# Performance work log

Hardware: AMD Instinct MI355X
Metric: run time of the kernel (lower is better)

## Reference

```python
import jax, jax.numpy as jnp
import numpy as np

DIM = 512
HEADS = 8
DIM_HEAD = 64
INNER = HEADS * DIM_HEAD  # 512
SCALE = DIM_HEAD ** -0.5
NEG = -jnp.finfo(jnp.float32).max


def setup_inputs() -> dict:
    key = jax.random.key(0)
    k1, k2, k3, k4, k5 = jax.random.split(key, 5)
    b, n = 2, 4096
    x = jax.random.normal(k1, (b, n, DIM), dtype=jnp.float32)
    mask = jnp.ones((b, n), dtype=bool)
    gamma = jnp.ones((DIM,), dtype=jnp.float32)
    # nn.Linear default init ~ U(-1/sqrt(fan_in), 1/sqrt(fan_in)); use scaled normal for simplicity
    Wq = jax.random.normal(k2, (DIM, INNER), dtype=jnp.float32) * (DIM ** -0.5)
    Wkv = jax.random.normal(k3, (DIM, 2 * INNER), dtype=jnp.float32) * (DIM ** -0.5)
    Wout = jax.random.normal(k4, (INNER, DIM), dtype=jnp.float32) * (INNER ** -0.5)
    return {"x": x, "mask": mask, "gamma": gamma, "Wq": Wq, "Wkv": Wkv, "Wout": Wout}


def _layer_norm(x, gamma):
    mu = jnp.mean(x, axis=-1, keepdims=True)
    var = jnp.var(x, axis=-1, keepdims=True)
    return (x - mu) * jax.lax.rsqrt(var + 1e-5) * gamma  # beta buffer is zeros


def reference(x, mask, gamma, Wq, Wkv, Wout):
    b, n, _ = x.shape
    xn = _layer_norm(x, gamma)
    q = xn @ Wq                      # [b,n,inner]
    kv = xn @ Wkv                    # [b,n,2*inner]
    k, v = jnp.split(kv, 2, axis=-1)
    # b n (h d) -> b h n d
    def split_heads(t):
        return t.reshape(b, n, HEADS, DIM_HEAD).transpose(0, 2, 1, 3)
    q, k, v = split_heads(q) * SCALE, split_heads(k), split_heads(v)
    sim = jnp.einsum('bhid,bhjd->bhij', q, k)  # [b,h,n,n]
    sim = jnp.where(mask[:, None, None, :], sim, NEG)
    causal = jnp.triu(jnp.ones((n, n), dtype=bool), k=1)
    sim = jnp.where(causal, NEG, sim)
    attn = jax.nn.softmax(sim, axis=-1)
    out = jnp.einsum('bhij,bhjd->bhid', attn, v)       # [b,h,n,d]
    out = out.transpose(0, 2, 1, 3).reshape(b, n, INNER)
    return out @ Wout
```

## Files before the change

kernel.cpp:

```cpp
#include <hip/hip_runtime.h>
#include <hip/hip_bf16.h>
#include <stdint.h>

typedef __attribute__((ext_vector_type(8))) short bf16x8;
typedef __attribute__((ext_vector_type(4))) short s16x4;
typedef __attribute__((ext_vector_type(4))) float f32x4;
typedef __attribute__((ext_vector_type(16))) float f32x16;
typedef __attribute__((ext_vector_type(4))) uint32_t u32x4;

__device__ __forceinline__ short f2bf(float f) {
    union { float f; uint32_t u; } v; v.f = f;
    uint32_t r = v.u + 0x7fffu + ((v.u >> 16) & 1u);
    return (short)(r >> 16);
}

__device__ __forceinline__ float bf2f(uint32_t bits) {
    union { uint32_t u; float f; } v; v.u = bits;
    return v.f;
}

__device__ __forceinline__ uint32_t cvtpk(float a, float b) {
    uint32_t r;
    asm("v_cvt_pk_bf16_f32 %0, %1, %2" : "=v"(r) : "v"(a), "v"(b));
    return r;
}

__device__ __forceinline__ void plswap(uint32_t& x, uint32_t& y) {
    asm volatile("v_permlane32_swap_b32 %0, %1" : "+v"(x), "+v"(y));
}

__device__ __forceinline__ f32x16 mfma32(bf16x8 a, bf16x8 b, f32x16 c) {
    return __builtin_amdgcn_mfma_f32_32x32x16_bf16(a, b, c, 0, 0, 0);
}

__device__ __forceinline__ void gload_lds16(const void* g, void* l) {
    __builtin_amdgcn_global_load_lds(
        (const __attribute__((address_space(1))) void*)g,
        (__attribute__((address_space(3))) void*)l, 16, 0, 0);
}

__global__ __launch_bounds__(256) void prep_ln(
    const float* __restrict__ x, const float* __restrict__ gamma,
    const float* __restrict__ Wq, const float* __restrict__ Wkv,
    const float* __restrict__ Wout, short* __restrict__ xn,
    short* __restrict__ WqkvT, short* __restrict__ WoutT) {
    if (blockIdx.x < 8192) {
        int row = blockIdx.x;
        const float* xr = x + (size_t)row * 512;
        float2 v = *(const float2*)(xr + threadIdx.x * 2);
        float s = v.x + v.y;
        float ss = v.x * v.x + v.y * v.y;
#pragma unroll
        for (int off = 1; off < 64; off <<= 1) {
            s += __shfl_xor(s, off);
            ss += __shfl_xor(ss, off);
        }
        __shared__ float sbuf[4], ssbuf[4];
        int wid = threadIdx.x >> 6;
        if ((threadIdx.x & 63) == 0) { sbuf[wid] = s; ssbuf[wid] = ss; }
        __syncthreads();
        s = sbuf[0] + sbuf[1] + sbuf[2] + sbuf[3];
        ss = ssbuf[0] + ssbuf[1] + ssbuf[2] + ssbuf[3];
        float mu = s * (1.f / 512.f);
        float var = ss * (1.f / 512.f) - mu * mu;
        float rstd = rsqrtf(var + 1e-5f);
        float2 g = *(const float2*)(gamma + threadIdx.x * 2);
        uint32_t lo = (uint16_t)f2bf((v.x - mu) * rstd * g.x);
        uint32_t hi = (uint16_t)f2bf((v.y - mu) * rstd * g.y);
        *(uint32_t*)(xn + (size_t)row * 512 + threadIdx.x * 2) = lo | (hi << 16);
    } else {
        int tid = (blockIdx.x - 8192) * 256 + threadIdx.x;
        if (tid < 1536 * 512) {
            int n = tid >> 9, k = tid & 511;
            float w = (n < 512) ? Wq[k * 512 + n] : Wkv[k * 1024 + (n - 512)];
            WqkvT[tid] = f2bf(w);
        } else {
            int t = tid - 1536 * 512;
            int n = t >> 9, k = t & 511;
            WoutT[t] = f2bf(Wout[k * 512 + n]);
        }
    }
}

template <int EPI>
__global__ __launch_bounds__(256) void gemm_bt(const short* __restrict__ A,
                                               const short* __restrict__ Bt,
                                               void* __restrict__ C,
                                               short* __restrict__ Vt) {
    constexpr int K = 512;
    __shared__ __align__(16) short As[128 * 64];
    __shared__ __align__(16) short Bs[128 * 64];
    const int tid = threadIdx.x;
    const int lane = tid & 63;
    const int wid = tid >> 6;
    const int m0 = blockIdx.x * 128;
    const int n0 = blockIdx.y * 128;
    const int wr = wid >> 1, wc = wid & 1;
    const int hi = lane >> 4, lo = lane & 15;

    f32x4 acc[4][4] = {};
    for (int kt = 0; kt < K / 64; ++kt) {
        __syncthreads();
#pragma unroll
        for (int r = 0; r < 4; ++r) {
            int c = (r * 4 + wid) * 64 + lane;
            int row = c >> 3, c8 = c & 7;
            int kcol = kt * 64 + ((c8 ^ (row & 7)) << 3);
            gload_lds16(A + (size_t)(m0 + row) * K + kcol,
                        (char*)As + (r * 4 + wid) * 1024);
            gload_lds16(Bt + (size_t)(n0 + row) * K + kcol,
                        (char*)Bs + (r * 4 + wid) * 1024);
        }
        __syncthreads();
#pragma unroll
        for (int kk = 0; kk < 2; ++kk) {
            bf16x8 af[4], bfr[4];
            int cc = hi + kk * 4;
#pragma unroll
            for (int i = 0; i < 4; ++i) {
                int row = wr * 64 + i * 16 + lo;
                af[i] = *(const bf16x8*)((const char*)As + row * 128 +
                                         ((cc ^ (row & 7)) << 4));
                int nrow = wc * 64 + i * 16 + lo;
                bfr[i] = *(const bf16x8*)((const char*)Bs + nrow * 128 +
                                          ((cc ^ (nrow & 7)) << 4));
            }
#pragma unroll
            for (int i = 0; i < 4; ++i)
#pragma unroll
                for (int j = 0; j < 4; ++j)
                    acc[i][j] = __builtin_amdgcn_mfma_f32_16x16x32_bf16(
                        af[i], bfr[j], acc[i][j], 0, 0, 0);
        }
    }
#pragma unroll
    for (int i = 0; i < 4; ++i)
#pragma unroll
        for (int j = 0; j < 4; ++j) {
            int col = n0 + wc * 64 + j * 16 + lo;
            int row0 = m0 + wr * 64 + i * 16 + hi * 4;
            if (EPI == 1) {
#pragma unroll
                for (int r = 0; r < 4; ++r)
                    ((float*)C)[(size_t)(row0 + r) * 512 + col] = acc[i][j][r];
            } else if (col < 1024) {
                float sc = (col < 512) ? 0.18033688011112042f : 1.0f;
#pragma unroll
                for (int r = 0; r < 4; ++r)
                    ((short*)C)[(size_t)(row0 + r) * 1536 + col] =
                        f2bf(acc[i][j][r] * sc);
            } else {
                s16x4 pk;
#pragma unroll
                for (int r = 0; r < 4; ++r) pk[r] = f2bf(acc[i][j][r]);
                int d = col - 1024;
                int bb = row0 >> 12, n = row0 & 4095;
                *(s16x4*)(Vt + ((size_t)(bb * 8 + (d >> 6)) * 64 + (d & 63)) *
                                   4096 +
                          n) = pk;
            }
        }
}

__global__ __launch_bounds__(256, 4) void flash_attn(
    const short* __restrict__ qkv, const short* __restrict__ Vt,
    short* __restrict__ attn_out) {
    __shared__ __align__(16) char smem[32768];
    const int tid = threadIdx.x, lane = tid & 63, w = tid >> 6;
    const int hi32 = lane >> 5, lq = lane & 31;
    const int bid = blockIdx.x;
    const int qt = 127 - (bid >> 4);
    const int bh = bid & 15, b = bh >> 3, h = bh & 7;
    const int q0 = qt * 32;
    const int qg = q0 + lq;
    const int swzK = (lq & 7) ^ ((lq >> 3) & 1);
    const int swzV = (lq >> 1) & 3;

    bf16x8 qb[4];
    {
        const short* qrow = qkv + (size_t)(b * 4096 + qg) * 1536 + h * 64;
#pragma unroll
        for (int ks = 0; ks < 4; ++ks)
            qb[ks] = *(const bf16x8*)(qrow + ks * 16 + hi32 * 8);
    }

    int offK[4], offV[4], ldsO[4];
#pragma unroll
    for (int r = 0; r < 4; ++r) {
        int idx = r * 64 + lane;
        int krow = idx >> 3, kc = idx & 7;
        int ksw = (krow & 7) ^ ((krow >> 3) & 1);
        offK[r] = krow * 1536 + ((kc ^ ksw) << 3);
        int vrow = idx >> 2, vc = idx & 3;
        offV[r] = vrow * 4096 + ((vc ^ ((vrow >> 1) & 3)) << 3);
        ldsO[r] = idx * 16;
    }
    char* mybuf = smem + w * 8192;
    const short* kps =
        qkv + (size_t)b * 4096 * 1536 + 512 + h * 64 + (size_t)w * 32 * 1536;
    const short* vps = Vt + (size_t)bh * 64 * 4096 + w * 32;

    f32x16 oA = {}, oB = {};
    float m_r = -3.0e38f, l_r = 0.f;
    const int T = qt + 1;

    if (w < T) {
#pragma unroll
        for (int r = 0; r < 4; ++r) {
            gload_lds16(kps + offK[r], mybuf + ldsO[r]);
            gload_lds16(vps + offV[r], mybuf + 4096 + ldsO[r]);
        }
        kps += (size_t)4 * 32 * 1536;
        vps += 4 * 32;
        for (int t = w; t < T; t += 4) {
            asm volatile("s_waitcnt vmcnt(0)" ::: "memory");
            f32x16 sA = {};
            __builtin_amdgcn_s_setprio(1);
#pragma unroll
            for (int ks = 0; ks < 4; ++ks) {
                int p = (2 * ks + hi32) ^ swzK;
                bf16x8 kf = *(const bf16x8*)(mybuf + lq * 128 + p * 16);
                sA = mfma32(kf, qb[ks], sA);
            }
            __builtin_amdgcn_s_setprio(0);
            bf16x8 vfA[2], vfB[2];
#pragma unroll
            for (int ks = 0; ks < 2; ++ks) {
                int p = (2 * ks + hi32) ^ swzV;
                vfA[ks] = *(const bf16x8*)(mybuf + 4096 + lq * 64 + p * 16);
                vfB[ks] =
                    *(const bf16x8*)(mybuf + 4096 + (lq + 32) * 64 + p * 16);
            }
            asm volatile("s_waitcnt lgkmcnt(0)" ::: "memory");
            __builtin_amdgcn_sched_barrier(0);
            if (t + 4 < T) {
#pragma unroll
                for (int r = 0; r < 4; ++r) {
                    gload_lds16(kps + offK[r], mybuf + ldsO[r]);
                    gload_lds16(vps + offV[r], mybuf + 4096 + ldsO[r]);
                }
                kps += (size_t)4 * 32 * 1536;
                vps += 4 * 32;
            }
            int kv0 = t * 32;
            if (kv0 + 31 > q0) {
                int c4 = 4 * hi32;
#pragma unroll
                for (int r2 = 0; r2 < 16; ++r2) {
                    int kvl = (r2 & 3) + 8 * (r2 >> 2) + c4;
                    sA[r2] = (kv0 + kvl > qg) ? -3.0e38f : sA[r2];
                }
            }
            float a0 = fmaxf(fmaxf(sA[0], sA[1]), sA[2]);
            float a1 = fmaxf(fmaxf(sA[3], sA[4]), sA[5]);
            float a2 = fmaxf(fmaxf(sA[6], sA[7]), sA[8]);
            float a3 = fmaxf(fmaxf(sA[9], sA[10]), sA[11]);
            float a4 = fmaxf(fmaxf(sA[12], sA[13]), sA[14]);
            float mt = fmaxf(fmaxf(fmaxf(a0, a1), a2),
                             fmaxf(fmaxf(a3, a4), sA[15]));
            mt = fmaxf(mt, __shfl_xor(mt, 32));
            if (!__all(mt <= m_r + 8.0f)) {
                float alpha = exp2f(m_r - mt);
                m_r = mt;
                l_r *= alpha;
#pragma unroll
                for (int r2 = 0; r2 < 16; ++r2) {
                    oA[r2] *= alpha;
                    oB[r2] *= alpha;
                }
            }
#pragma unroll
            for (int r2 = 0; r2 < 16; ++r2) sA[r2] = exp2f(sA[r2] - m_r);
            float sum0;
            {
                float s0 = (sA[0] + sA[1]) + (sA[2] + sA[3]);
                float s1 = (sA[4] + sA[5]) + (sA[6] + sA[7]);
                float s2 = (sA[8] + sA[9]) + (sA[10] + sA[11]);
                float s3 = (sA[12] + sA[13]) + (sA[14] + sA[15]);
                sum0 = (s0 + s1) + (s2 + s3);
            }
            l_r += sum0 + __shfl_xor(sum0, 32);
#pragma unroll
            for (int ks = 0; ks < 2; ++ks) {
                const int base = ks * 8;
                uint32_t x0 = cvtpk(sA[base + 0], sA[base + 1]);
                uint32_t y0 = cvtpk(sA[base + 4], sA[base + 5]);
                plswap(x0, y0);
                uint32_t x1 = cvtpk(sA[base + 2], sA[base + 3]);
                uint32_t y1 = cvtpk(sA[base + 6], sA[base + 7]);
                plswap(x1, y1);
                union { uint32_t wd[4]; bf16x8 v; } u;
                u.wd[0] = x0; u.wd[1] = x1; u.wd[2] = y0; u.wd[3] = y1;
                __builtin_amdgcn_s_setprio(1);
                oA = mfma32(vfA[ks], u.v, oA);
                oB = mfma32(vfB[ks], u.v, oB);
                __builtin_amdgcn_s_setprio(0);
            }
        }
    }
    __syncthreads();
    {
        char* epi = smem + w * 4224;
        float invl = (l_r > 0.f) ? (1.0f / l_r) : 0.f;
#pragma unroll
        for (int r2 = 0; r2 < 16; r2 += 2) {
            int wbase = ((r2 & 3) >> 1) + 4 * (r2 >> 2) + 2 * hi32;
            *(uint32_t*)(epi + lq * 132 + wbase * 4) =
                cvtpk(oA[r2] * invl, oA[r2 + 1] * invl);
            *(uint32_t*)(epi + lq * 132 + 64 + wbase * 4) =
                cvtpk(oB[r2] * invl, oB[r2 + 1] * invl);
        }
        float* mlb = (float*)(smem + 16896);
        if (hi32 == 0) {
            mlb[w * 64 + lq] = m_r;
            mlb[w * 64 + 32 + lq] = l_r;
        }
    }
    __syncthreads();
    {
        const int q = tid >> 3, dg = tid & 7;
        const float* mlb = (const float*)(smem + 16896);
        float M = -3.0e38f;
        float mm[4], ll[4];
#pragma unroll
        for (int s = 0; s < 4; ++s) {
            mm[s] = mlb[s * 64 + q];
            ll[s] = mlb[s * 64 + 32 + q];
            M = fmaxf(M, mm[s]);
        }
        float L = 0.f;
        float acc[8] = {};
#pragma unroll
        for (int s = 0; s < 4; ++s) {
            float a = exp2f(mm[s] - M) * ll[s];
            L += a;
            const uint32_t* p32 =
                (const uint32_t*)(smem + s * 4224 + q * 132 + dg * 16);
#pragma unroll
            for (int j = 0; j < 4; ++j) {
                uint32_t pv = p32[j];
                acc[2 * j] += a * bf2f(pv << 16);
                acc[2 * j + 1] += a * bf2f(pv & 0xffff0000u);
            }
        }
        float inv = 1.0f / L;
        u32x4 o;
#pragma unroll
        for (int j = 0; j < 4; ++j)
            o[j] = cvtpk(acc[2 * j] * inv, acc[2 * j + 1] * inv);
        uint32_t* attn32 = (uint32_t*)attn_out;
        *(u32x4*)(attn32 + (size_t)(b * 4096 + q0 + q) * 256 + h * 32 + dg * 4) =
            o;
    }
}

extern "C" void kernel_launch(void* const* d_in, const int* in_sizes, int n_in,
                              void* d_out, int out_size, void* d_ws,
                              size_t ws_size, hipStream_t stream) {
    const float* x = (const float*)d_in[0];
    const float* gamma = (const float*)d_in[2];
    const float* Wq = (const float*)d_in[3];
    const float* Wkv = (const float*)d_in[4];
    const float* Wout = (const float*)d_in[5];

    char* ws = (char*)d_ws;
    short* xn = (short*)(ws);
    short* qkv = (short*)(ws + (8ull << 20));
    short* Vt = (short*)(ws + (32ull << 20));
    short* attn = (short*)(ws + (40ull << 20));
    short* WqkvT = (short*)(ws + (48ull << 20));
    short* WoutT = (short*)(ws + (50ull << 20));

    prep_ln<<<12288, 256, 0, stream>>>(x, gamma, Wq, Wkv, Wout, xn, WqkvT,
                                       WoutT);
    gemm_bt<0><<<dim3(64, 12), 256, 0, stream>>>(xn, WqkvT, qkv, Vt);
    flash_attn<<<2048, 256, 0, stream>>>(qkv, Vt, attn);
    gemm_bt<1><<<dim3(64, 4), 256, 0, stream>>>(attn, WoutT, (float*)d_out,
                                                nullptr);
}
```

Measured before the change: 130.8 us.

## Process two 32-row query tiles per flash-attention block to reuse K/V loads

Each attention block now handles 64 query rows as two 32-row sub-tiles sharing every K/V tile staged in LDS. This halves the block count and the global K/V traffic per query. The price is more accumulator registers, so the launch-bounds occupancy hint drops from 4 to 3, and a two-phase epilogue is added. The first sub-tile skips fully masked KV tiles.

```diff
diff --git a/kernel.cpp b/kernel.cpp
--- a/kernel.cpp
+++ b/kernel.cpp
@@ -162,26 +162,28 @@
         }
 }
 
-__global__ __launch_bounds__(256, 4) void flash_attn(
+__global__ __launch_bounds__(256, 3) void flash_attn(
     const short* __restrict__ qkv, const short* __restrict__ Vt,
     short* __restrict__ attn_out) {
     __shared__ __align__(16) char smem[32768];
     const int tid = threadIdx.x, lane = tid & 63, w = tid >> 6;
     const int hi32 = lane >> 5, lq = lane & 31;
     const int bid = blockIdx.x;
-    const int qt = 127 - (bid >> 4);
+    const int s = 63 - (bid >> 4);
     const int bh = bid & 15, b = bh >> 3, h = bh & 7;
-    const int q0 = qt * 32;
-    const int qg = q0 + lq;
+    const int q0 = s * 64;
+    const int qgA = q0 + lq;
     const int swzK = (lq & 7) ^ ((lq >> 3) & 1);
     const int swzV = (lq >> 1) & 3;
 
-    bf16x8 qb[4];
+    bf16x8 qbA[4], qbB[4];
     {
-        const short* qrow = qkv + (size_t)(b * 4096 + qg) * 1536 + h * 64;
-#pragma unroll
-        for (int ks = 0; ks < 4; ++ks)
-            qb[ks] = *(const bf16x8*)(qrow + ks * 16 + hi32 * 8);
+        const short* qrowA = qkv + (size_t)(b * 4096 + qgA) * 1536 + h * 64;
+#pragma unroll
+        for (int ks = 0; ks < 4; ++ks) {
+            qbA[ks] = *(const bf16x8*)(qrowA + ks * 16 + hi32 * 8);
+            qbB[ks] = *(const bf16x8*)(qrowA + 32 * 1536 + ks * 16 + hi32 * 8);
+        }
     }
 
     int offK[4], offV[4], ldsO[4];
@@ -200,9 +202,10 @@
         qkv + (size_t)b * 4096 * 1536 + 512 + h * 64 + (size_t)w * 32 * 1536;
     const short* vps = Vt + (size_t)bh * 64 * 4096 + w * 32;
 
-    f32x16 oA = {}, oB = {};
-    float m_r = -3.0e38f, l_r = 0.f;
-    const int T = qt + 1;
+    f32x16 oAA = {}, oBA = {};
+    f32x16 oAB = {}, oBB = {};
+    float mA = -3.0e38f, lA = 0.f, mB = -3.0e38f, lB = 0.f;
+    const int T = 2 * s + 2;
 
     if (w < T) {
 #pragma unroll
@@ -213,14 +216,17 @@
         kps += (size_t)4 * 32 * 1536;
         vps += 4 * 32;
         for (int t = w; t < T; t += 4) {
+            const int kv0 = t * 32;
+            const bool doA = kv0 <= q0 + 31;
             asm volatile("s_waitcnt vmcnt(0)" ::: "memory");
-            f32x16 sA = {};
+            f32x16 sA = {}, sB = {};
             __builtin_amdgcn_s_setprio(1);
 #pragma unroll
             for (int ks = 0; ks < 4; ++ks) {
                 int p = (2 * ks + hi32) ^ swzK;
                 bf16x8 kf = *(const bf16x8*)(mybuf + lq * 128 + p * 16);
-                sA = mfma32(kf, qb[ks], sA);
+                sA = mfma32(kf, qbA[ks], sA);
+                sB = mfma32(kf, qbB[ks], sB);
             }
             __builtin_amdgcn_s_setprio(0);
             bf16x8 vfA[2], vfB[2];
@@ -242,115 +248,173 @@
                 kps += (size_t)4 * 32 * 1536;
                 vps += 4 * 32;
             }
-            int kv0 = t * 32;
-            if (kv0 + 31 > q0) {
-                int c4 = 4 * hi32;
-#pragma unroll
-                for (int r2 = 0; r2 < 16; ++r2) {
-                    int kvl = (r2 & 3) + 8 * (r2 >> 2) + c4;
-                    sA[r2] = (kv0 + kvl > qg) ? -3.0e38f : sA[r2];
-                }
-            }
-            float a0 = fmaxf(fmaxf(sA[0], sA[1]), sA[2]);
-            float a1 = fmaxf(fmaxf(sA[3], sA[4]), sA[5]);
-            float a2 = fmaxf(fmaxf(sA[6], sA[7]), sA[8]);
-            float a3 = fmaxf(fmaxf(sA[9], sA[10]), sA[11]);
-            float a4 = fmaxf(fmaxf(sA[12], sA[13]), sA[14]);
-            float mt = fmaxf(fmaxf(fmaxf(a0, a1), a2),
-                             fmaxf(fmaxf(a3, a4), sA[15]));
-            mt = fmaxf(mt, __shfl_xor(mt, 32));
-            if (!__all(mt <= m_r + 8.0f)) {
-                float alpha = exp2f(m_r - mt);
-                m_r = mt;
-                l_r *= alpha;
-#pragma unroll
-                for (int r2 = 0; r2 < 16; ++r2) {
-                    oA[r2] *= alpha;
-                    oB[r2] *= alpha;
-                }
-            }
-#pragma unroll
-            for (int r2 = 0; r2 < 16; ++r2) sA[r2] = exp2f(sA[r2] - m_r);
-            float sum0;
-            {
+            if (doA) {
+                if (kv0 + 31 > q0) {
+                    int c4 = 4 * hi32;
+#pragma unroll
+                    for (int r2 = 0; r2 < 16; ++r2) {
+                        int kvl = (r2 & 3) + 8 * (r2 >> 2) + c4;
+                        sA[r2] = (kv0 + kvl > qgA) ? -3.0e38f : sA[r2];
+                    }
+                }
+                float a0 = fmaxf(fmaxf(sA[0], sA[1]), sA[2]);
+                float a1 = fmaxf(fmaxf(sA[3], sA[4]), sA[5]);
+                float a2 = fmaxf(fmaxf(sA[6], sA[7]), sA[8]);
+                float a3 = fmaxf(fmaxf(sA[9], sA[10]), sA[11]);
+                float a4 = fmaxf(fmaxf(sA[12], sA[13]), sA[14]);
+                float mt = fmaxf(fmaxf(fmaxf(a0, a1), a2),
+                                 fmaxf(fmaxf(a3, a4), sA[15]));
+                mt = fmaxf(mt, __shfl_xor(mt, 32));
+                if (!__all(mt <= mA + 8.0f)) {
+                    float alpha = exp2f(mA - mt);
+                    mA = mt;
+                    lA *= alpha;
+#pragma unroll
+                    for (int r2 = 0; r2 < 16; ++r2) {
+                        oAA[r2] *= alpha;
+                        oBA[r2] *= alpha;
+                    }
+                }
+#pragma unroll
+                for (int r2 = 0; r2 < 16; ++r2) sA[r2] = exp2f(sA[r2] - mA);
                 float s0 = (sA[0] + sA[1]) + (sA[2] + sA[3]);
                 float s1 = (sA[4] + sA[5]) + (sA[6] + sA[7]);
                 float s2 = (sA[8] + sA[9]) + (sA[10] + sA[11]);
                 float s3 = (sA[12] + sA[13]) + (sA[14] + sA[15]);
-                sum0 = (s0 + s1) + (s2 + s3);
-            }
-            l_r += sum0 + __shfl_xor(sum0, 32);
-#pragma unroll
-            for (int ks = 0; ks < 2; ++ks) {
-                const int base = ks * 8;
-                uint32_t x0 = cvtpk(sA[base + 0], sA[base + 1]);
-                uint32_t y0 = cvtpk(sA[base + 4], sA[base + 5]);
-                plswap(x0, y0);
-                uint32_t x1 = cvtpk(sA[base + 2], sA[base + 3]);
-                uint32_t y1 = cvtpk(sA[base + 6], sA[base + 7]);
-                plswap(x1, y1);
-                union { uint32_t wd[4]; bf16x8 v; } u;
-                u.wd[0] = x0; u.wd[1] = x1; u.wd[2] = y0; u.wd[3] = y1;
-                __builtin_amdgcn_s_setprio(1);
-                oA = mfma32(vfA[ks], u.v, oA);
-                oB = mfma32(vfB[ks], u.v, oB);
-                __builtin_amdgcn_s_setprio(0);
-            }
-        }
-    }
-    __syncthreads();
-    {
-        char* epi = smem + w * 4224;
-        float invl = (l_r > 0.f) ? (1.0f / l_r) : 0.f;
-#pragma unroll
-        for (int r2 = 0; r2 < 16; r2 += 2) {
-            int wbase = ((r2 & 3) >> 1) + 4 * (r2 >> 2) + 2 * hi32;
-            *(uint32_t*)(epi + lq * 132 + wbase * 4) =
-                cvtpk(oA[r2] * invl, oA[r2 + 1] * invl);
-            *(uint32_t*)(epi + lq * 132 + 64 + wbase * 4) =
-                cvtpk(oB[r2] * invl, oB[r2 + 1] * invl);
-        }
-        float* mlb = (float*)(smem + 16896);
-        if (hi32 == 0) {
-            mlb[w * 64 + lq] = m_r;
-            mlb[w * 64 + 32 + lq] = l_r;
-        }
-    }
-    __syncthreads();
-    {
-        const int q = tid >> 3, dg = tid & 7;
-        const float* mlb = (const float*)(smem + 16896);
-        float M = -3.0e38f;
-        float mm[4], ll[4];
-#pragma unroll
-        for (int s = 0; s < 4; ++s) {
-            mm[s] = mlb[s * 64 + q];
-            ll[s] = mlb[s * 64 + 32 + q];
-            M = fmaxf(M, mm[s]);
-        }
-        float L = 0.f;
-        float acc[8] = {};
-#pragma unroll
-        for (int s = 0; s < 4; ++s) {
-            float a = exp2f(mm[s] - M) * ll[s];
-            L += a;
-            const uint32_t* p32 =
-                (const uint32_t*)(smem + s * 4224 + q * 132 + dg * 16);
-#pragma unroll
-            for (int j = 0; j < 4; ++j) {
-                uint32_t pv = p32[j];
-                acc[2 * j] += a * bf2f(pv << 16);
-                acc[2 * j + 1] += a * bf2f(pv & 0xffff0000u);
-            }
-        }
-        float inv = 1.0f / L;
-        u32x4 o;
-#pragma unroll
-        for (int j = 0; j < 4; ++j)
-            o[j] = cvtpk(acc[2 * j] * inv, acc[2 * j + 1] * inv);
-        uint32_t* attn32 = (uint32_t*)attn_out;
-        *(u32x4*)(attn32 + (size_t)(b * 4096 + q0 + q) * 256 + h * 32 + dg * 4) =
-            o;
+                float sum0 = (s0 + s1) + (s2 + s3);
+                lA += sum0 + __shfl_xor(sum0, 32);
+#pragma unroll
+                for (int ks = 0; ks < 2; ++ks) {
+                    const int base = ks * 8;
+                    uint32_t x0 = cvtpk(sA[base + 0], sA[base + 1]);
+                    uint32_t y0 = cvtpk(sA[base + 4], sA[base + 5]);
+                    plswap(x0, y0);
+                    uint32_t x1 = cvtpk(sA[base + 2], sA[base + 3]);
+                    uint32_t y1 = cvtpk(sA[base + 6], sA[base + 7]);
+                    plswap(x1, y1);
+                    union { uint32_t wd[4]; bf16x8 v; } u;
+                    u.wd[0] = x0; u.wd[1] = x1; u.wd[2] = y0; u.wd[3] = y1;
+                    __builtin_amdgcn_s_setprio(1);
+                    oAA = mfma32(vfA[ks], u.v, oAA);
+                    oBA = mfma32(vfB[ks], u.v, oBA);
+                    __builtin_amdgcn_s_setprio(0);
+                }
+            }
+            {
+                if (kv0 + 31 > q0 + 32) {
+                    int c4 = 4 * hi32;
+#pragma unroll
+                    for (int r2 = 0; r2 < 16; ++r2) {
+                        int kvl = (r2 & 3) + 8 * (r2 >> 2) + c4;
+                        sB[r2] = (kv0 + kvl > qgA + 32) ? -3.0e38f : sB[r2];
+                    }
+                }
+                float a0 = fmaxf(fmaxf(sB[0], sB[1]), sB[2]);
+                float a1 = fmaxf(fmaxf(sB[3], sB[4]), sB[5]);
+                float a2 = fmaxf(fmaxf(sB[6], sB[7]), sB[8]);
+                float a3 = fmaxf(fmaxf(sB[9], sB[10]), sB[11]);
+                float a4 = fmaxf(fmaxf(sB[12], sB[13]), sB[14]);
+                float mt = fmaxf(fmaxf(fmaxf(a0, a1), a2),
+                                 fmaxf(fmaxf(a3, a4), sB[15]));
+                mt = fmaxf(mt, __shfl_xor(mt, 32));
+                if (!__all(mt <= mB + 8.0f)) {
+                    float alpha = exp2f(mB - mt);
+                    mB = mt;
+                    lB *= alpha;
+#pragma unroll
+                    for (int r2 = 0; r2 < 16; ++r2) {
+                        oAB[r2] *= alpha;
+                        oBB[r2] *= alpha;
+                    }
+                }
+#pragma unroll
+                for (int r2 = 0; r2 < 16; ++r2) sB[r2] = exp2f(sB[r2] - mB);
+                float s0 = (sB[0] + sB[1]) + (sB[2] + sB[3]);
+                float s1 = (sB[4] + sB[5]) + (sB[6] + sB[7]);
+                float s2 = (sB[8] + sB[9]) + (sB[10] + sB[11]);
+                float s3 = (sB[12] + sB[13]) + (sB[14] + sB[15]);
+                float sum0 = (s0 + s1) + (s2 + s3);
+                lB += sum0 + __shfl_xor(sum0, 32);
+#pragma unroll
+                for (int ks = 0; ks < 2; ++ks) {
+                    const int base = ks * 8;
+                    uint32_t x0 = cvtpk(sB[base + 0], sB[base + 1]);
+                    uint32_t y0 = cvtpk(sB[base + 4], sB[base + 5]);
+                    plswap(x0, y0);
+                    uint32_t x1 = cvtpk(sB[base + 2], sB[base + 3]);
+                    uint32_t y1 = cvtpk(sB[base + 6], sB[base + 7]);
+                    plswap(x1, y1);
+                    union { uint32_t wd[4]; bf16x8 v; } u;
+                    u.wd[0] = x0; u.wd[1] = x1; u.wd[2] = y0; u.wd[3] = y1;
+                    __builtin_amdgcn_s_setprio(1);
+                    oAB = mfma32(vfA[ks], u.v, oAB);
+                    oBB = mfma32(vfB[ks], u.v, oBB);
+                    __builtin_amdgcn_s_setprio(0);
+                }
+            }
+        }
+    }
+    uint32_t* attn32 = (uint32_t*)attn_out;
+#pragma unroll
+    for (int phase = 0; phase < 2; ++phase) {
+        __syncthreads();
+        {
+            char* epi = smem + w * 4224;
+            float m_r = phase ? mB : mA;
+            float l_r = phase ? lB : lA;
+            const f32x16& o0 = phase ? oAB : oAA;
+            const f32x16& o1 = phase ? oBB : oBA;
+            float invl = (l_r > 0.f) ? (1.0f / l_r) : 0.f;
+#pragma unroll
+            for (int r2 = 0; r2 < 16; r2 += 2) {
+                int wbase = ((r2 & 3) >> 1) + 4 * (r2 >> 2) + 2 * hi32;
+                *(uint32_t*)(epi + lq * 132 + wbase * 4) =
+                    cvtpk(o0[r2] * invl, o0[r2 + 1] * invl);
+                *(uint32_t*)(epi + lq * 132 + 64 + wbase * 4) =
+                    cvtpk(o1[r2] * invl, o1[r2 + 1] * invl);
+            }
+            float* mlb = (float*)(smem + 16896);
+            if (hi32 == 0) {
+                mlb[w * 64 + lq] = m_r;
+                mlb[w * 64 + 32 + lq] = l_r;
+            }
+        }
+        __syncthreads();
+        {
+            const int q = tid >> 3, dg = tid & 7;
+            const float* mlb = (const float*)(smem + 16896);
+            float M = -3.0e38f;
+            float mm[4], ll[4];
+#pragma unroll
+            for (int ss = 0; ss < 4; ++ss) {
+                mm[ss] = mlb[ss * 64 + q];
+                ll[ss] = mlb[ss * 64 + 32 + q];
+                M = fmaxf(M, mm[ss]);
+            }
+            float L = 0.f;
+            float acc[8] = {};
+#pragma unroll
+            for (int ss = 0; ss < 4; ++ss) {
+                float a = exp2f(mm[ss] - M) * ll[ss];
+                L += a;
+                const uint32_t* p32 =
+                    (const uint32_t*)(smem + ss * 4224 + q * 132 + dg * 16);
+#pragma unroll
+                for (int j = 0; j < 4; ++j) {
+                    uint32_t pv = p32[j];
+                    acc[2 * j] += a * bf2f(pv << 16);
+                    acc[2 * j + 1] += a * bf2f(pv & 0xffff0000u);
+                }
+            }
+            float inv = 1.0f / L;
+            u32x4 o;
+#pragma unroll
+            for (int j = 0; j < 4; ++j)
+                o[j] = cvtpk(acc[2 * j] * inv, acc[2 * j + 1] * inv);
+            *(u32x4*)(attn32 +
+                      (size_t)(b * 4096 + q0 + phase * 32 + q) * 256 + h * 32 +
+                      dg * 4) = o;
+        }
     }
 }
 
@@ -374,7 +438,7 @@
     prep_ln<<<12288, 256, 0, stream>>>(x, gamma, Wq, Wkv, Wout, xn, WqkvT,
                                        WoutT);
     gemm_bt<0><<<dim3(64, 12), 256, 0, stream>>>(xn, WqkvT, qkv, Vt);
-    flash_attn<<<2048, 256, 0, stream>>>(qkv, Vt, attn);
+    flash_attn<<<1024, 256, 0, stream>>>(qkv, Vt, attn);
     gemm_bt<1><<<dim3(64, 4), 256, 0, stream>>>(attn, WoutT, (float*)d_out,
                                                 nullptr);
 }
```

Result: slower. 165.0 us (+26.2%).
